# Kernel tuning notes

Hardware: AMD Instinct MI355X
Metric: run time of the kernel (lower is better)

The kernel has to match this reference:

```python
import jax, jax.numpy as jnp
import numpy as np

N = 10000   # nodes
E = 80000   # edges
B = 2       # batch
T = 12      # time steps
F_IN = 64
F_OUT = 64


def setup_inputs() -> dict:
    key = jax.random.key(0)
    ks = jax.random.split(key, 8)
    x = jax.random.normal(ks[0], (B, N, T, F_IN), dtype=jnp.float32)
    src = jax.random.randint(ks[1], (E,), 0, N)
    dst = jax.random.randint(ks[2], (E,), 0, N)
    s = 1.0 / np.sqrt(F_IN)
    W_pool = jax.random.uniform(ks[3], (F_IN, F_IN), jnp.float32, -s, s)
    b_pool = jax.random.uniform(ks[4], (F_IN,), jnp.float32, -s, s)
    W_neigh = jax.random.uniform(ks[5], (F_OUT, F_IN), jnp.float32, -s, s)
    W_self = jax.random.uniform(ks[6], (F_OUT, F_IN), jnp.float32, -s, s)
    bias = jnp.zeros((F_OUT,), jnp.float32)
    return dict(x=x, src=src, dst=dst, W_pool=W_pool, b_pool=b_pool,
                W_neigh=W_neigh, W_self=W_self, bias=bias)


def reference(x, src, dst, W_pool, b_pool, W_neigh, W_self, bias):
    # x: (B, N, T, F) -> (N, B, T, F); node dim first as SAGEConv expects
    h = jnp.transpose(x, (1, 0, 2, 3))
    # pool aggregator: per-node MLP + relu (done on nodes, then gathered per edge
    # -- identical math to gather-then-MLP since the MLP is per-node/elementwise)
    msg = jax.nn.relu(jnp.einsum('nbtf,gf->nbtg', h, W_pool) + b_pool)  # (N,B,T,F)
    m = msg[src]                                                        # (E,B,T,F) gather
    neigh = jax.ops.segment_max(m, dst, num_segments=N)                 # max-pool per dst node
    # zero-in-degree nodes get -inf from segment_max -> replace with 0 (DGL behavior)
    neigh = jnp.where(jnp.isfinite(neigh), neigh, jnp.zeros((), neigh.dtype))
    rst = (jnp.einsum('nbtf,of->nbto', h, W_self)
           + jnp.einsum('nbtf,of->nbto', neigh, W_neigh)
           + bias)                                                      # (N,B,T,F_OUT)
    return jnp.transpose(rst, (1, 0, 2, 3))                              # (B,N,T,F_OUT)
```

## Files before the change

### kernel.cpp

```cpp
#include <hip/hip_runtime.h>

#define NN 10000
#define NE 80000
#define NB 2
#define NT 12
#define NF 64
#define ROWS (NB*NN*NT)

typedef __attribute__((ext_vector_type(8))) short bf16x8;
typedef __attribute__((ext_vector_type(2))) unsigned short u16x2;
typedef __attribute__((ext_vector_type(4))) float f32x4;
typedef __attribute__((ext_vector_type(4))) float fv4;

#define QCLAMP 4.0f
#define QSCALE 63.75f

__device__ __forceinline__ unsigned short f2b(float f) {
    unsigned int u = __builtin_bit_cast(unsigned int, f);
    u += 0x7fffu + ((u >> 16) & 1u);
    return (unsigned short)(u >> 16);
}
__device__ __forceinline__ unsigned pmax16(unsigned a, unsigned b) {
    u16x2 x = __builtin_bit_cast(u16x2, a), y = __builtin_bit_cast(u16x2, b);
    return __builtin_bit_cast(unsigned, __builtin_elementwise_max(x, y));
}

__global__ __launch_bounds__(256) void k_prep(const float* __restrict__ Wp,
        const float* __restrict__ Wn, const float* __restrict__ Ws,
        unsigned short* __restrict__ Wp_b, unsigned short* __restrict__ Wcat) {
    int t = threadIdx.x;
    for (int i = t; i < 4096; i += 256) {
        Wp_b[i] = f2b(Wp[i]);
        int o = i >> 6, g = i & 63;
        Wcat[o*128 + g] = f2b(Ws[i]);
        Wcat[o*128 + 64 + ((g & 15)*4 + (g >> 4))] = f2b(Wn[i] * (1.0f / QSCALE));
    }
}

__global__ __launch_bounds__(256) void k_msg(const float* __restrict__ x,
        const unsigned short* __restrict__ Wp_b, const float* __restrict__ bp,
        unsigned char* __restrict__ msg8, unsigned short* __restrict__ xb) {
    __shared__ __align__(16) unsigned short A[128*72];
    __shared__ __align__(16) unsigned short W[64*72];
    int tid = threadIdx.x;
    {
        int row = tid >> 2, c = (tid & 3) * 16;
        bf16x8 w0 = *(const bf16x8*)(Wp_b + row*64 + c);
        bf16x8 w1 = *(const bf16x8*)(Wp_b + row*64 + c + 8);
        *(bf16x8*)(W + row*72 + c)     = w0;
        *(bf16x8*)(W + row*72 + c + 8) = w1;
    }
    int m0 = blockIdx.x * 128;
    #pragma unroll
    for (int k = 0; k < 8; ++k) {
        int c = tid + 256*k;
        int row = c >> 4, f0 = (c & 15) * 4;
        int grow = m0 + row;
        fv4 v = __builtin_nontemporal_load((const fv4*)(x + (size_t)grow*64 + f0));
        uint2 p;
        p.x = f2b(v.x) | ((unsigned int)f2b(v.y) << 16);
        p.y = f2b(v.z) | ((unsigned int)f2b(v.w) << 16);
        *(uint2*)(A + row*72 + f0) = p;
        int b = grow / (NN*NT);
        int rem = grow - b*(NN*NT);
        int node = rem / NT, t = rem - node*NT;
        *(uint2*)(xb + ((size_t)node*24 + b*12 + t)*64 + f0) = p;
    }
    __syncthreads();

    int lane = tid & 63, w = tid >> 6;
    int cl = lane & 15, gq = lane >> 4;
    f32x4 acc[2][4] = {};
    #pragma unroll
    for (int kk = 0; kk < 2; ++kk) {
        int ko = kk*32 + gq*8;
        bf16x8 a0 = *(const bf16x8*)(A + (w*32 + cl)*72 + ko);
        bf16x8 a1 = *(const bf16x8*)(A + (w*32 + 16 + cl)*72 + ko);
        #pragma unroll
        for (int nf = 0; nf < 4; ++nf) {
            bf16x8 b = *(const bf16x8*)(W + (nf*16 + cl)*72 + ko);
            acc[0][nf] = __builtin_amdgcn_mfma_f32_16x16x32_bf16(a0, b, acc[0][nf], 0,0,0);
            acc[1][nf] = __builtin_amdgcn_mfma_f32_16x16x32_bf16(a1, b, acc[1][nf], 0,0,0);
        }
    }
    float bpv[4];
    #pragma unroll
    for (int nf = 0; nf < 4; ++nf) bpv[nf] = bp[nf*16 + cl];
    #pragma unroll
    for (int m = 0; m < 2; ++m)
    #pragma unroll
    for (int r = 0; r < 4; ++r) {
        int row = m0 + w*32 + m*16 + gq*4 + r;
        int b  = row / (NN*NT);
        int rem = row - b*(NN*NT);
        int node = rem / NT, t = rem - node*NT;
        unsigned q0 = (unsigned)(fminf(fmaxf(acc[m][0][r] + bpv[0], 0.f), QCLAMP)*QSCALE + 0.5f);
        unsigned q1 = (unsigned)(fminf(fmaxf(acc[m][1][r] + bpv[1], 0.f), QCLAMP)*QSCALE + 0.5f);
        unsigned q2 = (unsigned)(fminf(fmaxf(acc[m][2][r] + bpv[2], 0.f), QCLAMP)*QSCALE + 0.5f);
        unsigned q3 = (unsigned)(fminf(fmaxf(acc[m][3][r] + bpv[3], 0.f), QCLAMP)*QSCALE + 0.5f);
        *(unsigned*)(msg8 + ((size_t)(node*24 + b*12 + t) << 6) + cl*4) =
            q0 | (q1 << 8) | (q2 << 16) | (q3 << 24);
    }
}

__global__ void k_count(const int* __restrict__ dst, int* __restrict__ cnt) {
    int e = blockIdx.x * blockDim.x + threadIdx.x;
    if (e < NE) atomicAdd(&cnt[dst[e]], 1);
}

__global__ __launch_bounds__(1024) void k_scan(const int* __restrict__ cnt,
        int* __restrict__ rowptr, int* __restrict__ wofs) {
    __shared__ int s[1024];
    int tid = threadIdx.x;
    const int C = 10;
    int base = tid * C;
    int loc[C];
    int sum = 0;
    for (int i = 0; i < C; ++i) {
        int idx = base + i;
        int v = (idx < NN) ? cnt[idx] : 0;
        loc[i] = sum;
        sum += v;
    }
    s[tid] = sum;
    __syncthreads();
    for (int off = 1; off < 1024; off <<= 1) {
        int v = (tid >= off) ? s[tid - off] : 0;
        __syncthreads();
        s[tid] += v;
        __syncthreads();
    }
    int prev = (tid == 0) ? 0 : s[tid - 1];
    for (int i = 0; i < C; ++i) {
        int idx = base + i;
        if (idx < NN) {
            int v = prev + loc[i];
            rowptr[idx] = v;
            wofs[idx]   = v;
        }
    }
    if (tid == 1023) rowptr[NN] = s[1023];
}

__global__ void k_scatter(const int* __restrict__ src, const int* __restrict__ dst,
        int* __restrict__ wofs, int* __restrict__ csr) {
    int e = blockIdx.x * blockDim.x + threadIdx.x;
    if (e < NE) {
        int pos = atomicAdd(&wofs[dst[e]], 1);
        csr[pos] = src[e];
    }
}

__global__ __launch_bounds__(256, 4) void k_out(const unsigned short* __restrict__ xb,
        const unsigned char* __restrict__ msg8, const unsigned short* __restrict__ Wcat,
        const float* __restrict__ bias,
        const int* __restrict__ rowptr, const int* __restrict__ csr,
        float* __restrict__ out) {
    __shared__ __align__(16) unsigned short NL[4*24*72 + 8*72];
    int tid = threadIdx.x;
    int w = tid >> 6, lane = tid & 63;
    int n = blockIdx.x * 4 + w;
    unsigned short* tile = NL + w * (24*72);
    int cl = lane & 15, gq = lane >> 4;

    const unsigned short* xrow = xb + (size_t)n * 1536;
    bf16x8 a_self[2][2];
    #pragma unroll
    for (int kk = 0; kk < 2; ++kk) {
        int ko = kk*32 + gq*8;
        a_self[0][kk] = *(const bf16x8*)(xrow + cl*64 + ko);
        a_self[1][kk] = *(const bf16x8*)(xrow + (16 + cl)*64 + ko);
    }

    int rp0 = rowptr[n], rp1 = rowptr[n + 1];
    unsigned ae[6] = {0,0,0,0,0,0}, ao[6] = {0,0,0,0,0,0};
    #define ACC1(v, d) { ae[d] = pmax16(ae[d], (v) & 0x00FF00FFu); \
                         ao[d] = pmax16(ao[d], ((v) >> 8) & 0x00FF00FFu); }
    #define ACCE(a, b) { ACC1(a.x,0) ACC1(a.y,1) ACC1(a.z,2) ACC1(a.w,3) \
                         ACC1(b.x,4) ACC1(b.y,5) }
    int e = rp0;
    for (; e + 4 <= rp1; e += 4) {
        const char* p0 = (const char*)msg8 + (size_t)csr[e  ]*1536;
        const char* p1 = (const char*)msg8 + (size_t)csr[e+1]*1536;
        const char* p2 = (const char*)msg8 + (size_t)csr[e+2]*1536;
        const char* p3 = (const char*)msg8 + (size_t)csr[e+3]*1536;
        uint4 A0 = *(const uint4*)(p0 + lane*16), A1 = *(const uint4*)(p1 + lane*16);
        uint4 A2 = *(const uint4*)(p2 + lane*16), A3 = *(const uint4*)(p3 + lane*16);
        uint2 B0 = *(const uint2*)(p0 + 1024 + lane*8), B1 = *(const uint2*)(p1 + 1024 + lane*8);
        uint2 B2 = *(const uint2*)(p2 + 1024 + lane*8), B3 = *(const uint2*)(p3 + 1024 + lane*8);
        ACCE(A0, B0) ACCE(A1, B1) ACCE(A2, B2) ACCE(A3, B3)
    }
    for (; e < rp1; ++e) {
        const char* p0 = (const char*)msg8 + (size_t)csr[e]*1536;
        uint4 A0 = *(const uint4*)(p0 + lane*16);
        uint2 B0 = *(const uint2*)(p0 + 1024 + lane*8);
        ACCE(A0, B0)
    }
    {
        unsigned short t16[16];
        #pragma unroll
        for (int d = 0; d < 4; ++d) {
            t16[4*d+0] = f2b((float)(ae[d] & 0xFFu));
            t16[4*d+1] = f2b((float)(ao[d] & 0xFFu));
            t16[4*d+2] = f2b((float)(ae[d] >> 16));
            t16[4*d+3] = f2b((float)(ao[d] >> 16));
        }
        *(bf16x8*)(tile + (lane>>2)*72 + (lane&3)*16)     = *(bf16x8*)&t16[0];
        *(bf16x8*)(tile + (lane>>2)*72 + (lane&3)*16 + 8) = *(bf16x8*)&t16[8];
        unsigned short t8[8];
        #pragma unroll
        for (int d = 4; d < 6; ++d) {
            t8[4*(d-4)+0] = f2b((float)(ae[d] & 0xFFu));
            t8[4*(d-4)+1] = f2b((float)(ao[d] & 0xFFu));
            t8[4*(d-4)+2] = f2b((float)(ae[d] >> 16));
            t8[4*(d-4)+3] = f2b((float)(ao[d] >> 16));
        }
        *(bf16x8*)(tile + (16 + (lane>>3))*72 + (lane&7)*8) = *(bf16x8*)&t8[0];
    }

    f32x4 acc0[4] = {}, acc1[4] = {};
    #pragma unroll
    for (int kk = 0; kk < 4; ++kk) {
        bf16x8 a0, a1;
        if (kk < 2) { a0 = a_self[0][kk]; a1 = a_self[1][kk]; }
        else {
            int ko = (kk - 2)*32 + gq*8;
            a0 = *(const bf16x8*)(tile + cl*72 + ko);
            a1 = *(const bf16x8*)(tile + (16 + cl)*72 + ko);
        }
        #pragma unroll
        for (int cg = 0; cg < 4; ++cg) {
            bf16x8 b = *(const bf16x8*)(Wcat + (cg*16 + cl)*128 + kk*32 + gq*8);
            acc0[cg] = __builtin_amdgcn_mfma_f32_16x16x32_bf16(a0, b, acc0[cg], 0,0,0);
            acc1[cg] = __builtin_amdgcn_mfma_f32_16x16x32_bf16(a1, b, acc1[cg], 0,0,0);
        }
    }
    #pragma unroll
    for (int cg = 0; cg < 4; ++cg) {
        float bv = bias[cg*16 + cl];
        #pragma unroll
        for (int r = 0; r < 4; ++r) {
            int row = gq*4 + r;
            int b0 = row / 12, tt = row - b0*12;
            __builtin_nontemporal_store(acc0[cg][r] + bv,
                out + ((size_t)(b0*NN + n)*12 + tt)*64 + cg*16 + cl);
        }
    }
    if (gq < 2) {
        #pragma unroll
        for (int cg = 0; cg < 4; ++cg) {
            float bv = bias[cg*16 + cl];
            #pragma unroll
            for (int r = 0; r < 4; ++r) {
                int row = 16 + gq*4 + r;
                int b0 = row / 12, tt = row - b0*12;
                __builtin_nontemporal_store(acc1[cg][r] + bv,
                    out + ((size_t)(b0*NN + n)*12 + tt)*64 + cg*16 + cl);
            }
        }
    }
}

extern "C" void kernel_launch(void* const* d_in, const int* in_sizes, int n_in,
                              void* d_out, int out_size, void* d_ws, size_t ws_size,
                              hipStream_t stream) {
    const float* x    = (const float*)d_in[0];
    const int*   src  = (const int*)  d_in[1];
    const int*   dst  = (const int*)  d_in[2];
    const float* Wp   = (const float*)d_in[3];
    const float* bp   = (const float*)d_in[4];
    const float* Wn   = (const float*)d_in[5];
    const float* Wsf  = (const float*)d_in[6];
    const float* bias = (const float*)d_in[7];
    float* out = (float*)d_out;

    char* ws = (char*)d_ws;
    int*            cnt    = (int*)           (ws);
    int*            rowptr = (int*)           (ws + 40064);
    int*            wofs   = (int*)           (ws + 80128);
    int*            csr    = (int*)           (ws + 120192);
    unsigned short* Wp_b   = (unsigned short*)(ws + 440320);
    unsigned short* Wcat   = (unsigned short*)(ws + 448512);
    unsigned short* xb     = (unsigned short*)(ws + 464896);
    unsigned char*  msg8   = (unsigned char*) (ws + 31184896);

    hipMemsetAsync(cnt, 0, NN * sizeof(int), stream);
    k_prep   <<<1, 256, 0, stream>>>(Wp, Wn, Wsf, Wp_b, Wcat);
    k_msg    <<<ROWS/128, 256, 0, stream>>>(x, Wp_b, bp, msg8, xb);
    k_count  <<<(NE + 255) / 256, 256, 0, stream>>>(dst, cnt);
    k_scan   <<<1, 1024, 0, stream>>>(cnt, rowptr, wofs);
    k_scatter<<<(NE + 255) / 256, 256, 0, stream>>>(src, dst, wofs, csr);
    k_out    <<<NN/4, 256, 0, stream>>>(xb, msg8, Wcat, bias, rowptr, csr, out);
}
```

Measured before the change: 101.5 us.

## Fuse prep and count kernels, split each node's gather across four waves

Removes k_prep and k_count: the in-degree atomics and the Wp bf16 conversion move into k_msg, and the Wcat conversion moves into k_scan, cutting two launches. k_out now assigns one node per block. Its four waves split the neighbour edges, combine their partial max results through shared memory, and each wave computes one 16-column output group. This spreads the edge-gather latency of one node over four waves and lowers per-wave register use (launch bounds raised to 8), at the cost of two block barriers and more blocks.

Measured after the change: 101.0 us. Within noise of the previous version (-0.4%).

```diff
diff --git a/kernel.cpp b/kernel.cpp
--- a/kernel.cpp
+++ b/kernel.cpp
@@ -25,30 +25,28 @@
     return __builtin_bit_cast(unsigned, __builtin_elementwise_max(x, y));
 }
 
-__global__ __launch_bounds__(256) void k_prep(const float* __restrict__ Wp,
-        const float* __restrict__ Wn, const float* __restrict__ Ws,
-        unsigned short* __restrict__ Wp_b, unsigned short* __restrict__ Wcat) {
-    int t = threadIdx.x;
-    for (int i = t; i < 4096; i += 256) {
-        Wp_b[i] = f2b(Wp[i]);
-        int o = i >> 6, g = i & 63;
-        Wcat[o*128 + g] = f2b(Ws[i]);
-        Wcat[o*128 + 64 + ((g & 15)*4 + (g >> 4))] = f2b(Wn[i] * (1.0f / QSCALE));
-    }
-}
-
 __global__ __launch_bounds__(256) void k_msg(const float* __restrict__ x,
-        const unsigned short* __restrict__ Wp_b, const float* __restrict__ bp,
+        const float* __restrict__ Wp, const float* __restrict__ bp,
+        const int* __restrict__ dst, int* __restrict__ cnt,
         unsigned char* __restrict__ msg8, unsigned short* __restrict__ xb) {
     __shared__ __align__(16) unsigned short A[128*72];
     __shared__ __align__(16) unsigned short W[64*72];
     int tid = threadIdx.x;
     {
+        int e = blockIdx.x * 256 + tid;
+        if (e < NE) atomicAdd(&cnt[dst[e]], 1);
+    }
+    {
         int row = tid >> 2, c = (tid & 3) * 16;
-        bf16x8 w0 = *(const bf16x8*)(Wp_b + row*64 + c);
-        bf16x8 w1 = *(const bf16x8*)(Wp_b + row*64 + c + 8);
-        *(bf16x8*)(W + row*72 + c)     = w0;
-        *(bf16x8*)(W + row*72 + c + 8) = w1;
+        unsigned short ws16[16];
+        #pragma unroll
+        for (int i = 0; i < 4; ++i) {
+            fv4 v = *(const fv4*)(Wp + row*64 + c + i*4);
+            ws16[i*4+0] = f2b(v.x); ws16[i*4+1] = f2b(v.y);
+            ws16[i*4+2] = f2b(v.z); ws16[i*4+3] = f2b(v.w);
+        }
+        *(bf16x8*)(W + row*72 + c)     = *(bf16x8*)&ws16[0];
+        *(bf16x8*)(W + row*72 + c + 8) = *(bf16x8*)&ws16[8];
     }
     int m0 = blockIdx.x * 128;
     #pragma unroll
@@ -103,15 +101,17 @@
     }
 }
 
-__global__ void k_count(const int* __restrict__ dst, int* __restrict__ cnt) {
-    int e = blockIdx.x * blockDim.x + threadIdx.x;
-    if (e < NE) atomicAdd(&cnt[dst[e]], 1);
-}
-
 __global__ __launch_bounds__(1024) void k_scan(const int* __restrict__ cnt,
-        int* __restrict__ rowptr, int* __restrict__ wofs) {
+        int* __restrict__ rowptr, int* __restrict__ wofs,
+        const float* __restrict__ Wn, const float* __restrict__ Ws,
+        unsigned short* __restrict__ Wcat) {
+    int tid = threadIdx.x;
+    for (int i = tid; i < 4096; i += 1024) {
+        int o = i >> 6, g = i & 63;
+        Wcat[o*128 + g] = f2b(Ws[i]);
+        Wcat[o*128 + 64 + ((g & 15)*4 + (g >> 4))] = f2b(Wn[i] * (1.0f / QSCALE));
+    }
     __shared__ int s[1024];
-    int tid = threadIdx.x;
     const int C = 10;
     int base = tid * C;
     int loc[C];
@@ -151,16 +151,16 @@
     }
 }
 
-__global__ __launch_bounds__(256, 4) void k_out(const unsigned short* __restrict__ xb,
+__global__ __launch_bounds__(256, 8) void k_out(const unsigned short* __restrict__ xb,
         const unsigned char* __restrict__ msg8, const unsigned short* __restrict__ Wcat,
         const float* __restrict__ bias,
         const int* __restrict__ rowptr, const int* __restrict__ csr,
         float* __restrict__ out) {
-    __shared__ __align__(16) unsigned short NL[4*24*72 + 8*72];
+    __shared__ __align__(16) unsigned char P[4*1536];
+    __shared__ __align__(16) unsigned short tile[32*72];
     int tid = threadIdx.x;
     int w = tid >> 6, lane = tid & 63;
-    int n = blockIdx.x * 4 + w;
-    unsigned short* tile = NL + w * (24*72);
+    int n = blockIdx.x;
     int cl = lane & 15, gq = lane >> 4;
 
     const unsigned short* xrow = xb + (size_t)n * 1536;
@@ -178,47 +178,55 @@
                          ao[d] = pmax16(ao[d], ((v) >> 8) & 0x00FF00FFu); }
     #define ACCE(a, b) { ACC1(a.x,0) ACC1(a.y,1) ACC1(a.z,2) ACC1(a.w,3) \
                          ACC1(b.x,4) ACC1(b.y,5) }
-    int e = rp0;
-    for (; e + 4 <= rp1; e += 4) {
-        const char* p0 = (const char*)msg8 + (size_t)csr[e  ]*1536;
-        const char* p1 = (const char*)msg8 + (size_t)csr[e+1]*1536;
-        const char* p2 = (const char*)msg8 + (size_t)csr[e+2]*1536;
-        const char* p3 = (const char*)msg8 + (size_t)csr[e+3]*1536;
+    int e = rp0 + w;
+    for (; e + 4 < rp1; e += 8) {
+        const char* p0 = (const char*)msg8 + (size_t)csr[e]*1536;
+        const char* p1 = (const char*)msg8 + (size_t)csr[e+4]*1536;
         uint4 A0 = *(const uint4*)(p0 + lane*16), A1 = *(const uint4*)(p1 + lane*16);
-        uint4 A2 = *(const uint4*)(p2 + lane*16), A3 = *(const uint4*)(p3 + lane*16);
         uint2 B0 = *(const uint2*)(p0 + 1024 + lane*8), B1 = *(const uint2*)(p1 + 1024 + lane*8);
-        uint2 B2 = *(const uint2*)(p2 + 1024 + lane*8), B3 = *(const uint2*)(p3 + 1024 + lane*8);
-        ACCE(A0, B0) ACCE(A1, B1) ACCE(A2, B2) ACCE(A3, B3)
-    }
-    for (; e < rp1; ++e) {
+        ACCE(A0, B0) ACCE(A1, B1)
+    }
+    if (e < rp1) {
         const char* p0 = (const char*)msg8 + (size_t)csr[e]*1536;
         uint4 A0 = *(const uint4*)(p0 + lane*16);
         uint2 B0 = *(const uint2*)(p0 + 1024 + lane*8);
         ACCE(A0, B0)
     }
     {
-        unsigned short t16[16];
-        #pragma unroll
-        for (int d = 0; d < 4; ++d) {
-            t16[4*d+0] = f2b((float)(ae[d] & 0xFFu));
-            t16[4*d+1] = f2b((float)(ao[d] & 0xFFu));
-            t16[4*d+2] = f2b((float)(ae[d] >> 16));
-            t16[4*d+3] = f2b((float)(ao[d] >> 16));
-        }
-        *(bf16x8*)(tile + (lane>>2)*72 + (lane&3)*16)     = *(bf16x8*)&t16[0];
-        *(bf16x8*)(tile + (lane>>2)*72 + (lane&3)*16 + 8) = *(bf16x8*)&t16[8];
-        unsigned short t8[8];
-        #pragma unroll
-        for (int d = 4; d < 6; ++d) {
-            t8[4*(d-4)+0] = f2b((float)(ae[d] & 0xFFu));
-            t8[4*(d-4)+1] = f2b((float)(ao[d] & 0xFFu));
-            t8[4*(d-4)+2] = f2b((float)(ae[d] >> 16));
-            t8[4*(d-4)+3] = f2b((float)(ao[d] >> 16));
-        }
-        *(bf16x8*)(tile + (16 + (lane>>3))*72 + (lane&7)*8) = *(bf16x8*)&t8[0];
-    }
-
-    f32x4 acc0[4] = {}, acc1[4] = {};
+        uint4 q0;
+        q0.x = ae[0] | (ao[0] << 8); q0.y = ae[1] | (ao[1] << 8);
+        q0.z = ae[2] | (ao[2] << 8); q0.w = ae[3] | (ao[3] << 8);
+        *(uint4*)(P + w*1536 + lane*16) = q0;
+        uint2 q1;
+        q1.x = ae[4] | (ao[4] << 8); q1.y = ae[5] | (ao[5] << 8);
+        *(uint2*)(P + w*1536 + 1024 + lane*8) = q1;
+    }
+    __syncthreads();
+
+    if (tid < 192) {
+        const unsigned* Pd = (const unsigned*)P;
+        #pragma unroll
+        for (int j = 0; j < 2; ++j) {
+            int d = tid*2 + j;
+            unsigned v0 = Pd[d], v1 = Pd[384 + d], v2 = Pd[768 + d], v3 = Pd[1152 + d];
+            unsigned fe = pmax16(pmax16(v0 & 0x00FF00FFu, v1 & 0x00FF00FFu),
+                                 pmax16(v2 & 0x00FF00FFu, v3 & 0x00FF00FFu));
+            unsigned fo = pmax16(pmax16((v0 >> 8) & 0x00FF00FFu, (v1 >> 8) & 0x00FF00FFu),
+                                 pmax16((v2 >> 8) & 0x00FF00FFu, (v3 >> 8) & 0x00FF00FFu));
+            unsigned short s0 = f2b((float)(fe & 0xFFu));
+            unsigned short s1 = f2b((float)(fo & 0xFFu));
+            unsigned short s2 = f2b((float)(fe >> 16));
+            unsigned short s3 = f2b((float)(fo >> 16));
+            int row = d >> 4, c4 = (d & 15) * 4;
+            uint2 o2;
+            o2.x = (unsigned)s0 | ((unsigned)s1 << 16);
+            o2.y = (unsigned)s2 | ((unsigned)s3 << 16);
+            *(uint2*)(tile + row*72 + c4) = o2;
+        }
+    }
+    __syncthreads();
+
+    f32x4 acc0 = {}, acc1 = {};
     #pragma unroll
     for (int kk = 0; kk < 4; ++kk) {
         bf16x8 a0, a1;
@@ -228,35 +236,25 @@
             a0 = *(const bf16x8*)(tile + cl*72 + ko);
             a1 = *(const bf16x8*)(tile + (16 + cl)*72 + ko);
         }
-        #pragma unroll
-        for (int cg = 0; cg < 4; ++cg) {
-            bf16x8 b = *(const bf16x8*)(Wcat + (cg*16 + cl)*128 + kk*32 + gq*8);
-            acc0[cg] = __builtin_amdgcn_mfma_f32_16x16x32_bf16(a0, b, acc0[cg], 0,0,0);
-            acc1[cg] = __builtin_amdgcn_mfma_f32_16x16x32_bf16(a1, b, acc1[cg], 0,0,0);
-        }
-    }
-    #pragma unroll
-    for (int cg = 0; cg < 4; ++cg) {
-        float bv = bias[cg*16 + cl];
+        bf16x8 b = *(const bf16x8*)(Wcat + (w*16 + cl)*128 + kk*32 + gq*8);
+        acc0 = __builtin_amdgcn_mfma_f32_16x16x32_bf16(a0, b, acc0, 0,0,0);
+        acc1 = __builtin_amdgcn_mfma_f32_16x16x32_bf16(a1, b, acc1, 0,0,0);
+    }
+    float bv = bias[w*16 + cl];
+    #pragma unroll
+    for (int r = 0; r < 4; ++r) {
+        int row = gq*4 + r;
+        int b0 = row / 12, tt = row - b0*12;
+        __builtin_nontemporal_store(acc0[r] + bv,
+            out + ((size_t)(b0*NN + n)*12 + tt)*64 + w*16 + cl);
+    }
+    if (gq < 2) {
         #pragma unroll
         for (int r = 0; r < 4; ++r) {
-            int row = gq*4 + r;
+            int row = 16 + gq*4 + r;
             int b0 = row / 12, tt = row - b0*12;
-            __builtin_nontemporal_store(acc0[cg][r] + bv,
-                out + ((size_t)(b0*NN + n)*12 + tt)*64 + cg*16 + cl);
-        }
-    }
-    if (gq < 2) {
-        #pragma unroll
-        for (int cg = 0; cg < 4; ++cg) {
-            float bv = bias[cg*16 + cl];
-            #pragma unroll
-            for (int r = 0; r < 4; ++r) {
-                int row = 16 + gq*4 + r;
-                int b0 = row / 12, tt = row - b0*12;
-                __builtin_nontemporal_store(acc1[cg][r] + bv,
-                    out + ((size_t)(b0*NN + n)*12 + tt)*64 + cg*16 + cl);
-            }
+            __builtin_nontemporal_store(acc1[r] + bv,
+                out + ((size_t)(b0*NN + n)*12 + tt)*64 + w*16 + cl);
         }
     }
 }
@@ -279,16 +277,13 @@
     int*            rowptr = (int*)           (ws + 40064);
     int*            wofs   = (int*)           (ws + 80128);
     int*            csr    = (int*)           (ws + 120192);
-    unsigned short* Wp_b   = (unsigned short*)(ws + 440320);
     unsigned short* Wcat   = (unsigned short*)(ws + 448512);
     unsigned short* xb     = (unsigned short*)(ws + 464896);
     unsigned char*  msg8   = (unsigned char*) (ws + 31184896);
 
     hipMemsetAsync(cnt, 0, NN * sizeof(int), stream);
-    k_prep   <<<1, 256, 0, stream>>>(Wp, Wn, Wsf, Wp_b, Wcat);
-    k_msg    <<<ROWS/128, 256, 0, stream>>>(x, Wp_b, bp, msg8, xb);
-    k_count  <<<(NE + 255) / 256, 256, 0, stream>>>(dst, cnt);
-    k_scan   <<<1, 1024, 0, stream>>>(cnt, rowptr, wofs);
+    k_msg    <<<ROWS/128, 256, 0, stream>>>(x, Wp, bp, dst, cnt, msg8, xb);
+    k_scan   <<<1, 1024, 0, stream>>>(cnt, rowptr, wofs, Wn, Wsf, Wcat);
     k_scatter<<<(NE + 255) / 256, 256, 0, stream>>>(src, dst, wofs, csr);
-    k_out    <<<NN/4, 256, 0, stream>>>(xb, msg8, Wcat, bias, rowptr, csr, out);
-}
+    k_out    <<<NN, 256, 0, stream>>>(xb, msg8, Wcat, bias, rowptr, csr, out);
+}
```

## Fuse weight prep and degree counting into other kernels; widen gather unroll

Applied to the files above, without the earlier changes.

Removes the separate k_prep and k_count launches. Wp is converted to bf16 inside each k_msg block, in-degree counting runs in the first blocks of k_msg, and the Wcat packing moves into k_scan. This cuts two kernel launches and their serialization gaps. The neighbor max-gather in k_out now handles 8 edges per iteration, padding the tail by repeating the last edge, and uses nontemporal loads to raise memory-level parallelism. Every k_msg block now does redundant Wp conversion, and the padded tail issues extra loads on low-degree nodes.

After: 110.0 us. 1.08x slower.

```diff
diff --git a/kernel.cpp b/kernel.cpp
--- a/kernel.cpp
+++ b/kernel.cpp
@@ -11,6 +11,8 @@
 typedef __attribute__((ext_vector_type(2))) unsigned short u16x2;
 typedef __attribute__((ext_vector_type(4))) float f32x4;
 typedef __attribute__((ext_vector_type(4))) float fv4;
+typedef __attribute__((ext_vector_type(4))) unsigned int u32x4;
+typedef __attribute__((ext_vector_type(2))) unsigned int u32x2;
 
 #define QCLAMP 4.0f
 #define QSCALE 63.75f
@@ -25,30 +27,28 @@
     return __builtin_bit_cast(unsigned, __builtin_elementwise_max(x, y));
 }
 
-__global__ __launch_bounds__(256) void k_prep(const float* __restrict__ Wp,
-        const float* __restrict__ Wn, const float* __restrict__ Ws,
-        unsigned short* __restrict__ Wp_b, unsigned short* __restrict__ Wcat) {
-    int t = threadIdx.x;
-    for (int i = t; i < 4096; i += 256) {
-        Wp_b[i] = f2b(Wp[i]);
-        int o = i >> 6, g = i & 63;
-        Wcat[o*128 + g] = f2b(Ws[i]);
-        Wcat[o*128 + 64 + ((g & 15)*4 + (g >> 4))] = f2b(Wn[i] * (1.0f / QSCALE));
-    }
-}
-
 __global__ __launch_bounds__(256) void k_msg(const float* __restrict__ x,
-        const unsigned short* __restrict__ Wp_b, const float* __restrict__ bp,
+        const float* __restrict__ Wp, const float* __restrict__ bp,
+        const int* __restrict__ dst, int* __restrict__ cnt,
         unsigned char* __restrict__ msg8, unsigned short* __restrict__ xb) {
     __shared__ __align__(16) unsigned short A[128*72];
     __shared__ __align__(16) unsigned short W[64*72];
     int tid = threadIdx.x;
     {
+        int e = blockIdx.x * 256 + tid;
+        if (e < NE) atomicAdd(&cnt[dst[e]], 1);
+    }
+    {
         int row = tid >> 2, c = (tid & 3) * 16;
-        bf16x8 w0 = *(const bf16x8*)(Wp_b + row*64 + c);
-        bf16x8 w1 = *(const bf16x8*)(Wp_b + row*64 + c + 8);
-        *(bf16x8*)(W + row*72 + c)     = w0;
-        *(bf16x8*)(W + row*72 + c + 8) = w1;
+        unsigned short ws16[16];
+        #pragma unroll
+        for (int i = 0; i < 4; ++i) {
+            fv4 v = *(const fv4*)(Wp + row*64 + c + i*4);
+            ws16[i*4+0] = f2b(v.x); ws16[i*4+1] = f2b(v.y);
+            ws16[i*4+2] = f2b(v.z); ws16[i*4+3] = f2b(v.w);
+        }
+        *(bf16x8*)(W + row*72 + c)     = *(bf16x8*)&ws16[0];
+        *(bf16x8*)(W + row*72 + c + 8) = *(bf16x8*)&ws16[8];
     }
     int m0 = blockIdx.x * 128;
     #pragma unroll
@@ -103,15 +103,17 @@
     }
 }
 
-__global__ void k_count(const int* __restrict__ dst, int* __restrict__ cnt) {
-    int e = blockIdx.x * blockDim.x + threadIdx.x;
-    if (e < NE) atomicAdd(&cnt[dst[e]], 1);
-}
-
 __global__ __launch_bounds__(1024) void k_scan(const int* __restrict__ cnt,
-        int* __restrict__ rowptr, int* __restrict__ wofs) {
+        int* __restrict__ rowptr, int* __restrict__ wofs,
+        const float* __restrict__ Wn, const float* __restrict__ Ws,
+        unsigned short* __restrict__ Wcat) {
+    int tid = threadIdx.x;
+    for (int i = tid; i < 4096; i += 1024) {
+        int o = i >> 6, g = i & 63;
+        Wcat[o*128 + g] = f2b(Ws[i]);
+        Wcat[o*128 + 64 + ((g & 15)*4 + (g >> 4))] = f2b(Wn[i] * (1.0f / QSCALE));
+    }
     __shared__ int s[1024];
-    int tid = threadIdx.x;
     const int C = 10;
     int base = tid * C;
     int loc[C];
@@ -178,42 +180,66 @@
                          ao[d] = pmax16(ao[d], ((v) >> 8) & 0x00FF00FFu); }
     #define ACCE(a, b) { ACC1(a.x,0) ACC1(a.y,1) ACC1(a.z,2) ACC1(a.w,3) \
                          ACC1(b.x,4) ACC1(b.y,5) }
-    int e = rp0;
-    for (; e + 4 <= rp1; e += 4) {
-        const char* p0 = (const char*)msg8 + (size_t)csr[e  ]*1536;
-        const char* p1 = (const char*)msg8 + (size_t)csr[e+1]*1536;
-        const char* p2 = (const char*)msg8 + (size_t)csr[e+2]*1536;
-        const char* p3 = (const char*)msg8 + (size_t)csr[e+3]*1536;
-        uint4 A0 = *(const uint4*)(p0 + lane*16), A1 = *(const uint4*)(p1 + lane*16);
-        uint4 A2 = *(const uint4*)(p2 + lane*16), A3 = *(const uint4*)(p3 + lane*16);
-        uint2 B0 = *(const uint2*)(p0 + 1024 + lane*8), B1 = *(const uint2*)(p1 + 1024 + lane*8);
-        uint2 B2 = *(const uint2*)(p2 + 1024 + lane*8), B3 = *(const uint2*)(p3 + 1024 + lane*8);
-        ACCE(A0, B0) ACCE(A1, B1) ACCE(A2, B2) ACCE(A3, B3)
-    }
-    for (; e < rp1; ++e) {
-        const char* p0 = (const char*)msg8 + (size_t)csr[e]*1536;
-        uint4 A0 = *(const uint4*)(p0 + lane*16);
-        uint2 B0 = *(const uint2*)(p0 + 1024 + lane*8);
-        ACCE(A0, B0)
+    if (rp1 > rp0) {
+        int last = rp1 - 1;
+        for (int e = rp0; e < rp1; e += 8) {
+            int i0 = csr[(e+0 < rp1) ? e+0 : last];
+            int i1 = csr[(e+1 < rp1) ? e+1 : last];
+            int i2 = csr[(e+2 < rp1) ? e+2 : last];
+            int i3 = csr[(e+3 < rp1) ? e+3 : last];
+            int i4 = csr[(e+4 < rp1) ? e+4 : last];
+            int i5 = csr[(e+5 < rp1) ? e+5 : last];
+            int i6 = csr[(e+6 < rp1) ? e+6 : last];
+            int i7 = csr[(e+7 < rp1) ? e+7 : last];
+            const unsigned char* p0 = msg8 + (size_t)i0*1536;
+            const unsigned char* p1 = msg8 + (size_t)i1*1536;
+            const unsigned char* p2 = msg8 + (size_t)i2*1536;
+            const unsigned char* p3 = msg8 + (size_t)i3*1536;
+            const unsigned char* p4 = msg8 + (size_t)i4*1536;
+            const unsigned char* p5 = msg8 + (size_t)i5*1536;
+            const unsigned char* p6 = msg8 + (size_t)i6*1536;
+            const unsigned char* p7 = msg8 + (size_t)i7*1536;
+            u32x4 A0 = __builtin_nontemporal_load((const u32x4*)(p0 + lane*16));
+            u32x4 A1 = __builtin_nontemporal_load((const u32x4*)(p1 + lane*16));
+            u32x4 A2 = __builtin_nontemporal_load((const u32x4*)(p2 + lane*16));
+            u32x4 A3 = __builtin_nontemporal_load((const u32x4*)(p3 + lane*16));
+            u32x4 A4 = __builtin_nontemporal_load((const u32x4*)(p4 + lane*16));
+            u32x4 A5 = __builtin_nontemporal_load((const u32x4*)(p5 + lane*16));
+            u32x4 A6 = __builtin_nontemporal_load((const u32x4*)(p6 + lane*16));
+            u32x4 A7 = __builtin_nontemporal_load((const u32x4*)(p7 + lane*16));
+            u32x2 B0 = __builtin_nontemporal_load((const u32x2*)(p0 + 1024 + lane*8));
+            u32x2 B1 = __builtin_nontemporal_load((const u32x2*)(p1 + 1024 + lane*8));
+            u32x2 B2 = __builtin_nontemporal_load((const u32x2*)(p2 + 1024 + lane*8));
+            u32x2 B3 = __builtin_nontemporal_load((const u32x2*)(p3 + 1024 + lane*8));
+            u32x2 B4 = __builtin_nontemporal_load((const u32x2*)(p4 + 1024 + lane*8));
+            u32x2 B5 = __builtin_nontemporal_load((const u32x2*)(p5 + 1024 + lane*8));
+            u32x2 B6 = __builtin_nontemporal_load((const u32x2*)(p6 + 1024 + lane*8));
+            u32x2 B7 = __builtin_nontemporal_load((const u32x2*)(p7 + 1024 + lane*8));
+            ACCE(A0, B0) ACCE(A1, B1) ACCE(A2, B2) ACCE(A3, B3)
+            ACCE(A4, B4) ACCE(A5, B5) ACCE(A6, B6) ACCE(A7, B7)
+        }
     }
     {
         unsigned short t16[16];
+        unsigned fe, fo;
         #pragma unroll
         for (int d = 0; d < 4; ++d) {
-            t16[4*d+0] = f2b((float)(ae[d] & 0xFFu));
-            t16[4*d+1] = f2b((float)(ao[d] & 0xFFu));
-            t16[4*d+2] = f2b((float)(ae[d] >> 16));
-            t16[4*d+3] = f2b((float)(ao[d] >> 16));
+            fe = ae[d]; fo = ao[d];
+            t16[4*d+0] = f2b((float)(fe & 0xFFu));
+            t16[4*d+1] = f2b((float)(fo & 0xFFu));
+            t16[4*d+2] = f2b((float)(fe >> 16));
+            t16[4*d+3] = f2b((float)(fo >> 16));
         }
         *(bf16x8*)(tile + (lane>>2)*72 + (lane&3)*16)     = *(bf16x8*)&t16[0];
         *(bf16x8*)(tile + (lane>>2)*72 + (lane&3)*16 + 8) = *(bf16x8*)&t16[8];
         unsigned short t8[8];
         #pragma unroll
         for (int d = 4; d < 6; ++d) {
-            t8[4*(d-4)+0] = f2b((float)(ae[d] & 0xFFu));
-            t8[4*(d-4)+1] = f2b((float)(ao[d] & 0xFFu));
-            t8[4*(d-4)+2] = f2b((float)(ae[d] >> 16));
-            t8[4*(d-4)+3] = f2b((float)(ao[d] >> 16));
+            fe = ae[d]; fo = ao[d];
+            t8[4*(d-4)+0] = f2b((float)(fe & 0xFFu));
+            t8[4*(d-4)+1] = f2b((float)(fo & 0xFFu));
+            t8[4*(d-4)+2] = f2b((float)(fe >> 16));
+            t8[4*(d-4)+3] = f2b((float)(fo >> 16));
         }
         *(bf16x8*)(tile + (16 + (lane>>3))*72 + (lane&7)*8) = *(bf16x8*)&t8[0];
     }
@@ -279,16 +305,13 @@
     int*            rowptr = (int*)           (ws + 40064);
     int*            wofs   = (int*)           (ws + 80128);
     int*            csr    = (int*)           (ws + 120192);
-    unsigned short* Wp_b   = (unsigned short*)(ws + 440320);
     unsigned short* Wcat   = (unsigned short*)(ws + 448512);
     unsigned short* xb     = (unsigned short*)(ws + 464896);
     unsigned char*  msg8   = (unsigned char*) (ws + 31184896);
 
     hipMemsetAsync(cnt, 0, NN * sizeof(int), stream);
-    k_prep   <<<1, 256, 0, stream>>>(Wp, Wn, Wsf, Wp_b, Wcat);
-    k_msg    <<<ROWS/128, 256, 0, stream>>>(x, Wp_b, bp, msg8, xb);
-    k_count  <<<(NE + 255) / 256, 256, 0, stream>>>(dst, cnt);
-    k_scan   <<<1, 1024, 0, stream>>>(cnt, rowptr, wofs);
+    k_msg    <<<ROWS/128, 256, 0, stream>>>(x, Wp, bp, dst, cnt, msg8, xb);
+    k_scan   <<<1, 1024, 0, stream>>>(cnt, rowptr, wofs, Wn, Wsf, Wcat);
     k_scatter<<<(NE + 255) / 256, 256, 0, stream>>>(src, dst, wofs, csr);
     k_out    <<<NN/4, 256, 0, stream>>>(xb, msg8, Wcat, bias, rowptr, csr, out);
 }
```
